# Kernel optimization log

Hardware: AMD Instinct MI355X
Metric: run time of the kernel (lower is better)

Reference implementation:

```python
import jax, jax.numpy as jnp
import numpy as np

EMBED_DIM = 128
NUM_HEADS = 4
HEAD_DIM = EMBED_DIM // NUM_HEADS


def setup_inputs() -> dict:
    key = jax.random.key(0)
    ks = jax.random.split(key, 12)
    B, N, D = 4, 4096, EMBED_DIM
    s = 1.0 / np.sqrt(D)
    inp = {
        "query": jax.random.normal(ks[0], (B, N, D), dtype=jnp.float32),
        "key": jax.random.normal(ks[1], (B, N, D), dtype=jnp.float32),
        "value": jax.random.normal(ks[2], (B, N, D), dtype=jnp.float32),
        "Wq": jax.random.uniform(ks[3], (D, D), jnp.float32, -s, s),
        "bq": jax.random.uniform(ks[4], (D,), jnp.float32, -s, s),
        "Wk": jax.random.uniform(ks[5], (D, D), jnp.float32, -s, s),
        "bk": jax.random.uniform(ks[6], (D,), jnp.float32, -s, s),
        "Wv": jax.random.uniform(ks[7], (D, D), jnp.float32, -s, s),
        "bv": jax.random.uniform(ks[8], (D,), jnp.float32, -s, s),
        "Wo": jax.random.uniform(ks[9], (D, D), jnp.float32, -s, s),
        "bo": jax.random.uniform(ks[10], (D,), jnp.float32, -s, s),
    }
    return inp


def reference(query, key, value, Wq, bq, Wk, bk, Wv, bv, Wo, bo):
    B, N, D = query.shape
    H, Dh = NUM_HEADS, HEAD_DIM
    scale = Dh ** -0.5
    # Linear projections (torch Linear: x @ W.T + b), split heads -> [B, H, N, Dh]
    Q = (query @ Wq.T + bq).reshape(B, N, H, Dh).transpose(0, 2, 1, 3)
    K = (key @ Wk.T + bk).reshape(B, N, H, Dh).transpose(0, 2, 1, 3)
    V = (value @ Wv.T + bv).reshape(B, N, H, Dh).transpose(0, 2, 1, 3)
    # Attention scores [B, H, N, N]
    scores = jnp.einsum('bhqd,bhkd->bhqk', Q, K) * scale
    attn = jax.nn.softmax(scores, axis=-1)
    ctx = jnp.einsum('bhqk,bhkd->bhqd', attn, V)  # [B, H, N, Dh]
    ctx = ctx.transpose(0, 2, 1, 3).reshape(B, N, D)
    return ctx @ Wo.T + bo
```

## Files before the change

kernel.cpp:

```cpp
#include <hip/hip_runtime.h>
#include <hip/hip_bf16.h>

#define N_SEQ 4096
#define DIM   128
#define NH    4
#define DH    32
#define BATCH 4

#define QSCALE 0.25503495870989204f

typedef __bf16 bf16x8 __attribute__((ext_vector_type(8)));
typedef __bf16 bf16x2 __attribute__((ext_vector_type(2)));
typedef __bf16 bf16x4 __attribute__((ext_vector_type(4)));
typedef float  f32x4  __attribute__((ext_vector_type(4)));

#define MFMA(a, b, c) __builtin_amdgcn_mfma_f32_16x16x32_bf16((a), (b), (c), 0, 0, 0)

static __device__ __forceinline__ bf16x8 cvt8(const float* __restrict__ p) {
    const float4* f4 = reinterpret_cast<const float4*>(p);
    float4 a = f4[0], b = f4[1];
    bf16x8 r;
    r[0] = (__bf16)a.x; r[1] = (__bf16)a.y; r[2] = (__bf16)a.z; r[3] = (__bf16)a.w;
    r[4] = (__bf16)b.x; r[5] = (__bf16)b.y; r[6] = (__bf16)b.z; r[7] = (__bf16)b.w;
    return r;
}

static __device__ __forceinline__ f32x4 exp4(f32x4 s) {
    f32x4 r;
    r[0] = __builtin_amdgcn_exp2f(s[0]);
    r[1] = __builtin_amdgcn_exp2f(s[1]);
    r[2] = __builtin_amdgcn_exp2f(s[2]);
    r[3] = __builtin_amdgcn_exp2f(s[3]);
    return r;
}

static __device__ __forceinline__ bf16x8 pack8(f32x4 a, f32x4 b) {
    bf16x8 o;
    o[0] = (__bf16)a[0]; o[1] = (__bf16)a[1];
    o[2] = (__bf16)a[2]; o[3] = (__bf16)a[3];
    o[4] = (__bf16)b[0]; o[5] = (__bf16)b[1];
    o[6] = (__bf16)b[2]; o[7] = (__bf16)b[3];
    return o;
}

__global__ __launch_bounds__(256) void proj_qkv(
    const float* __restrict__ xq, const float* __restrict__ xk, const float* __restrict__ xv,
    const float* __restrict__ Wq, const float* __restrict__ Wk, const float* __restrict__ Wv,
    const float* __restrict__ bq, const float* __restrict__ bk, const float* __restrict__ bv,
    __bf16* __restrict__ Qs, __bf16* __restrict__ Kb, __bf16* __restrict__ Vt)
{
    __shared__ __align__(16) char wlds[34816];
    const int z = blockIdx.z;
    const float* x    = (z == 0) ? xq : ((z == 1) ? xk : xv);
    const float* Wf   = (z == 0) ? Wq : ((z == 1) ? Wk : Wv);
    const float* bias = (z == 0) ? bq : ((z == 1) ? bk : bv);
    const int b    = blockIdx.y;
    const int tid  = threadIdx.x;
    const int wave = tid >> 6, lane = tid & 63;
    const int quad = lane >> 4, l15 = lane & 15;
    const int n0   = blockIdx.x * 64 + wave * 16;

    {
        const int r = tid >> 1, half = tid & 1;
        const float* wsrc = Wf + r * DIM + half * 64;
        char* wdst = wlds + r * 272 + half * 128;
        #pragma unroll
        for (int i = 0; i < 8; i++)
            *(bf16x8*)(wdst + i * 16) = cvt8(wsrc + i * 8);
    }

    bf16x8 a[4];
    const float* xrow = x + (b * N_SEQ + n0 + l15) * DIM + quad * 8;
    a[0] = cvt8(xrow);      a[1] = cvt8(xrow + 32);
    a[2] = cvt8(xrow + 64); a[3] = cvt8(xrow + 96);
    __syncthreads();

    const int n = n0 + l15;
    for (int t = 0; t < 8; t++) {
        const char* wr = wlds + (t * 16 + l15) * 272 + quad * 16;
        bf16x8 w0 = *(const bf16x8*)(wr);
        bf16x8 w1 = *(const bf16x8*)(wr + 64);
        bf16x8 w2 = *(const bf16x8*)(wr + 128);
        bf16x8 w3 = *(const bf16x8*)(wr + 192);

        f32x4 acc = {0.f, 0.f, 0.f, 0.f};
        acc = MFMA(w0, a[0], acc);
        acc = MFMA(w1, a[1], acc);
        acc = MFMA(w2, a[2], acc);
        acc = MFMA(w3, a[3], acc);

        const int d0 = t * 16 + quad * 4;
        if (z == 0) {
            const int h = d0 >> 5, dh0 = d0 & 31;
            bf16x4 q4;
            #pragma unroll
            for (int r = 0; r < 4; r++)
                q4[r] = (__bf16)((acc[r] + bias[d0 + r]) * QSCALE);
            *(bf16x4*)(Qs + ((b * NH + h) * N_SEQ + n) * DH + dh0) = q4;
        } else if (z == 1) {
            const int h = d0 >> 5, dh0 = d0 & 31;
            bf16x4 k4;
            #pragma unroll
            for (int r = 0; r < 4; r++)
                k4[r] = (__bf16)(acc[r] + bias[d0 + r]);
            *(bf16x4*)(Kb + ((b * NH + h) * N_SEQ + n) * DH + dh0) = k4;
        } else {
            const int nl = n & 63;
            const int np = (n & ~63) | (nl & 35) | ((nl & 12) << 1) | ((nl & 16) >> 2);
            #pragma unroll
            for (int r = 0; r < 4; r++) {
                const int d = d0 + r, h = d >> 5, dh = d & 31;
                Vt[((b * NH + h) * DH + dh) * N_SEQ + np] = (__bf16)(acc[r] + bias[d]);
            }
        }
    }
}

__global__ __launch_bounds__(256, 2) void flash_attn(
    const __bf16* __restrict__ Qs, const __bf16* __restrict__ Kb,
    const __bf16* __restrict__ Vt, __bf16* __restrict__ ctxb)
{
    __shared__ __align__(16) char smem[20480];
    char* const Kbase = smem;
    char* const Vbase = smem + 10240;

    const int bid  = blockIdx.x;
    const int bh   = bid & 15;
    const int qc   = bid >> 4;
    const int tid  = threadIdx.x;
    const int wave = tid >> 6, lane = tid & 63;
    const int quad = lane >> 4, l15 = lane & 15;
    const int n0   = qc * 128 + wave * 32;

    const __bf16* Qp = Qs + (bh * N_SEQ + n0) * DH;
    bf16x8 qf0 = *(const bf16x8*)(Qp + l15 * DH + quad * 8);
    bf16x8 qf1 = *(const bf16x8*)(Qp + (16 + l15) * DH + quad * 8);

    const int r_ = tid >> 2, c_ = tid & 3;
    const __bf16* gK = Kb + (size_t)bh * N_SEQ * DH + r_ * DH + c_ * 8;
    const int vd = ((r_ >> 4) & 1) * 16 + (r_ & 15);
    const int vg = r_ >> 5;
    const __bf16* gV = Vt + ((size_t)bh * DH + vd) * N_SEQ + vg * 32 + c_ * 8;
    const int kofs = r_ * 80 + c_ * 16;

    {
        bf16x8 kr = *(const bf16x8*)(gK);
        bf16x8 vr = *(const bf16x8*)(gV);
        *(bf16x8*)(Kbase + kofs) = kr;
        *(bf16x8*)(Vbase + kofs) = vr;
    }
    __syncthreads();

    f32x4 c00 = {0.f,0.f,0.f,0.f}, c01 = {0.f,0.f,0.f,0.f};
    f32x4 c10 = {0.f,0.f,0.f,0.f}, c11 = {0.f,0.f,0.f,0.f};
    f32x4 lac0 = {0.f,0.f,0.f,0.f}, lac1 = {0.f,0.f,0.f,0.f};
    const f32x4 z4 = {0.f,0.f,0.f,0.f};
    bf16x8 ones;
    #pragma unroll
    for (int i = 0; i < 8; i++) ones[i] = (__bf16)1.0f;

    for (int kb = 0; kb < N_SEQ / 64; kb++) {
        const int cur = kb & 1;
        const char* Kc = Kbase + cur * 5120;
        const char* Vc = Vbase + cur * 5120;

        const int kn = (kb + 1) & (N_SEQ / 64 - 1);
        bf16x8 krn = *(const bf16x8*)(gK + kn * 64 * DH);
        bf16x8 vrn = *(const bf16x8*)(gV + kn * 64);

        bf16x8 kf0 = *(const bf16x8*)(Kc + l15 * 80 + quad * 16);
        bf16x8 kf1 = *(const bf16x8*)(Kc + (16 + l15) * 80 + quad * 16);
        bf16x8 kf2 = *(const bf16x8*)(Kc + (32 + l15) * 80 + quad * 16);
        bf16x8 kf3 = *(const bf16x8*)(Kc + (48 + l15) * 80 + quad * 16);

        f32x4 s00 = MFMA(kf0, qf0, z4), s10 = MFMA(kf1, qf0, z4);
        f32x4 s20 = MFMA(kf2, qf0, z4), s30 = MFMA(kf3, qf0, z4);
        f32x4 s01 = MFMA(kf0, qf1, z4), s11 = MFMA(kf1, qf1, z4);
        f32x4 s21 = MFMA(kf2, qf1, z4), s31 = MFMA(kf3, qf1, z4);

        bf16x8 pf00 = pack8(exp4(s00), exp4(s10));
        bf16x8 pf10 = pack8(exp4(s20), exp4(s30));
        bf16x8 pf01 = pack8(exp4(s01), exp4(s11));
        bf16x8 pf11 = pack8(exp4(s21), exp4(s31));

        lac0 = MFMA(ones, pf00, lac0); lac0 = MFMA(ones, pf10, lac0);
        lac1 = MFMA(ones, pf01, lac1); lac1 = MFMA(ones, pf11, lac1);

        bf16x8 vf00 = *(const bf16x8*)(Vc + l15 * 80 + quad * 16);
        bf16x8 vf10 = *(const bf16x8*)(Vc + (16 + l15) * 80 + quad * 16);
        bf16x8 vf01 = *(const bf16x8*)(Vc + (32 + l15) * 80 + quad * 16);
        bf16x8 vf11 = *(const bf16x8*)(Vc + (48 + l15) * 80 + quad * 16);

        c00 = MFMA(vf00, pf00, c00); c01 = MFMA(vf10, pf00, c01);
        c00 = MFMA(vf01, pf10, c00); c01 = MFMA(vf11, pf10, c01);
        c10 = MFMA(vf00, pf01, c10); c11 = MFMA(vf10, pf01, c11);
        c10 = MFMA(vf01, pf11, c10); c11 = MFMA(vf11, pf11, c11);

        *(bf16x8*)(Kbase + (cur ^ 1) * 5120 + kofs) = krn;
        *(bf16x8*)(Vbase + (cur ^ 1) * 5120 + kofs) = vrn;
        __syncthreads();
    }

    const float inv0 = 1.0f / lac0[0];
    const float inv1 = 1.0f / lac1[0];

    const int b = bh >> 2, h = bh & 3;
    #pragma unroll
    for (int qt = 0; qt < 2; qt++) {
        const float inv = qt ? inv1 : inv0;
        const int q = n0 + qt * 16 + l15;
        #pragma unroll
        for (int dt = 0; dt < 2; dt++) {
            f32x4 cc = qt ? (dt ? c11 : c10) : (dt ? c01 : c00);
            __bf16* dst = ctxb + ((size_t)(b * N_SEQ + q)) * DIM + h * DH + dt * 16 + quad * 4;
            bf16x2 e0 = {(__bf16)(cc[0] * inv), (__bf16)(cc[1] * inv)};
            bf16x2 e1 = {(__bf16)(cc[2] * inv), (__bf16)(cc[3] * inv)};
            *(bf16x2*)(dst)     = e0;
            *(bf16x2*)(dst + 2) = e1;
        }
    }
}

__global__ __launch_bounds__(256) void out_proj(
    const __bf16* __restrict__ ctxb, const float* __restrict__ Wo,
    const float* __restrict__ bo, float* __restrict__ out)
{
    __shared__ __align__(16) char wlds[34816];
    const int b    = blockIdx.y;
    const int tid  = threadIdx.x;
    const int wave = tid >> 6, lane = tid & 63;
    const int quad = lane >> 4, l15 = lane & 15;
    const int n0   = blockIdx.x * 64 + wave * 16;

    {
        const int r = tid >> 1, half = tid & 1;
        const float* wsrc = Wo + r * DIM + half * 64;
        char* wdst = wlds + r * 272 + half * 128;
        #pragma unroll
        for (int i = 0; i < 8; i++)
            *(bf16x8*)(wdst + i * 16) = cvt8(wsrc + i * 8);
    }

    bf16x8 a[4];
    const __bf16* crow = ctxb + (b * N_SEQ + n0 + l15) * DIM + quad * 8;
    a[0] = *(const bf16x8*)(crow);
    a[1] = *(const bf16x8*)(crow + 32);
    a[2] = *(const bf16x8*)(crow + 64);
    a[3] = *(const bf16x8*)(crow + 96);
    __syncthreads();

    const int n = n0 + l15;
    for (int t = 0; t < 8; t++) {
        const char* wr = wlds + (t * 16 + l15) * 272 + quad * 16;
        bf16x8 w0 = *(const bf16x8*)(wr);
        bf16x8 w1 = *(const bf16x8*)(wr + 64);
        bf16x8 w2 = *(const bf16x8*)(wr + 128);
        bf16x8 w3 = *(const bf16x8*)(wr + 192);

        f32x4 acc = {0.f, 0.f, 0.f, 0.f};
        acc = MFMA(w0, a[0], acc);
        acc = MFMA(w1, a[1], acc);
        acc = MFMA(w2, a[2], acc);
        acc = MFMA(w3, a[3], acc);

        const int d0 = t * 16 + quad * 4;
        float4 o;
        o.x = acc[0] + bo[d0];
        o.y = acc[1] + bo[d0 + 1];
        o.z = acc[2] + bo[d0 + 2];
        o.w = acc[3] + bo[d0 + 3];
        *(float4*)(out + (b * N_SEQ + n) * DIM + d0) = o;
    }
}

extern "C" void kernel_launch(void* const* d_in, const int* in_sizes, int n_in,
                              void* d_out, int out_size, void* d_ws, size_t ws_size,
                              hipStream_t stream)
{
    const float* query = (const float*)d_in[0];
    const float* key   = (const float*)d_in[1];
    const float* value = (const float*)d_in[2];
    const float* Wq = (const float*)d_in[3];
    const float* bq = (const float*)d_in[4];
    const float* Wk = (const float*)d_in[5];
    const float* bk = (const float*)d_in[6];
    const float* Wv = (const float*)d_in[7];
    const float* bv = (const float*)d_in[8];
    const float* Wo = (const float*)d_in[9];
    const float* bo = (const float*)d_in[10];
    float* out = (float*)d_out;

    char* ws = (char*)d_ws;
    const size_t e = (size_t)BATCH * N_SEQ * DIM;
    __bf16* Qs   = (__bf16*)(ws);
    __bf16* Kb   = (__bf16*)(ws + 2 * e);
    __bf16* Vt   = (__bf16*)(ws + 4 * e);
    __bf16* ctxb = (__bf16*)(ws + 6 * e);

    proj_qkv<<<dim3(64, BATCH, 3), 256, 0, stream>>>(
        query, key, value, Wq, Wk, Wv, bq, bk, bv, Qs, Kb, Vt);
    flash_attn<<<dim3(512), 256, 0, stream>>>(Qs, Kb, Vt, ctxb);
    out_proj<<<dim3(64, BATCH), 256, 0, stream>>>(ctxb, Wo, bo, out);
}
```

Before: 160.2 us.

## Split key range across wave pairs with 64-query tiles and LDS reduction

Flash attention now gives each wave 64 query rows instead of 32. The four waves are split into two query halves times two key halves, and each key half walks 2048 keys. Partial context and row sums are merged through LDS at the end, and the row-sum MFMA with a ones vector is replaced by scalar adds plus lane shuffles. The aim is to reuse each K/V fragment across more queries and to halve the serial loop length, at the cost of more LDS (57 KB, which may limit occupancy to fewer blocks per CU), more registers and an extra reduction step.

Result: faster. 150.2 us (-6.3%).

```diff
diff --git a/kernel.cpp b/kernel.cpp
--- a/kernel.cpp
+++ b/kernel.cpp
@@ -120,9 +120,10 @@
     const __bf16* __restrict__ Qs, const __bf16* __restrict__ Kb,
     const __bf16* __restrict__ Vt, __bf16* __restrict__ ctxb)
 {
-    __shared__ __align__(16) char smem[20480];
+    __shared__ __align__(16) char smem[57344];
     char* const Kbase = smem;
-    char* const Vbase = smem + 10240;
+    char* const Vbase = smem + 20480;
+    char* const Pbase = smem + 38912;
 
     const int bid  = blockIdx.x;
     const int bh   = bid & 15;
@@ -130,93 +131,128 @@
     const int tid  = threadIdx.x;
     const int wave = tid >> 6, lane = tid & 63;
     const int quad = lane >> 4, l15 = lane & 15;
-    const int n0   = qc * 128 + wave * 32;
+    const int qh   = wave & 1, kh = wave >> 1;
+    const int n0   = qc * 128 + qh * 64;
 
     const __bf16* Qp = Qs + (bh * N_SEQ + n0) * DH;
-    bf16x8 qf0 = *(const bf16x8*)(Qp + l15 * DH + quad * 8);
-    bf16x8 qf1 = *(const bf16x8*)(Qp + (16 + l15) * DH + quad * 8);
+    bf16x8 qf[4];
+    #pragma unroll
+    for (int q = 0; q < 4; q++)
+        qf[q] = *(const bf16x8*)(Qp + (q * 16 + l15) * DH + quad * 8);
 
     const int r_ = tid >> 2, c_ = tid & 3;
     const __bf16* gK = Kb + (size_t)bh * N_SEQ * DH + r_ * DH + c_ * 8;
-    const int vd = ((r_ >> 4) & 1) * 16 + (r_ & 15);
-    const int vg = r_ >> 5;
-    const __bf16* gV = Vt + ((size_t)bh * DH + vd) * N_SEQ + vg * 32 + c_ * 8;
-    const int kofs = r_ * 80 + c_ * 16;
+    const __bf16* gV = Vt + ((size_t)bh * DH + (tid >> 3)) * N_SEQ + (tid & 7) * 8;
+    const int kofsK = r_ * 80 + c_ * 16;
+    const int kofsV = (tid >> 3) * 144 + (tid & 7) * 16;
+    const int KH = 2048;
 
     {
-        bf16x8 kr = *(const bf16x8*)(gK);
-        bf16x8 vr = *(const bf16x8*)(gV);
-        *(bf16x8*)(Kbase + kofs) = kr;
-        *(bf16x8*)(Vbase + kofs) = vr;
+        bf16x8 k0 = *(const bf16x8*)(gK);
+        bf16x8 k1 = *(const bf16x8*)(gK + (size_t)KH * DH);
+        bf16x8 v0 = *(const bf16x8*)(gV);
+        bf16x8 v1 = *(const bf16x8*)(gV + KH);
+        *(bf16x8*)(Kbase + kofsK)          = k0;
+        *(bf16x8*)(Kbase + 10240 + kofsK)  = k1;
+        *(bf16x8*)(Vbase + kofsV)          = v0;
+        *(bf16x8*)(Vbase + 9216 + kofsV)   = v1;
     }
     __syncthreads();
 
-    f32x4 c00 = {0.f,0.f,0.f,0.f}, c01 = {0.f,0.f,0.f,0.f};
-    f32x4 c10 = {0.f,0.f,0.f,0.f}, c11 = {0.f,0.f,0.f,0.f};
-    f32x4 lac0 = {0.f,0.f,0.f,0.f}, lac1 = {0.f,0.f,0.f,0.f};
+    char* const Kme = Kbase + kh * 10240;
+    char* const Vme = Vbase + kh * 9216;
+
+    f32x4 c[4][2];
+    #pragma unroll
+    for (int q = 0; q < 4; q++) { c[q][0] = f32x4{0.f,0.f,0.f,0.f}; c[q][1] = f32x4{0.f,0.f,0.f,0.f}; }
+    float l[4] = {0.f, 0.f, 0.f, 0.f};
     const f32x4 z4 = {0.f,0.f,0.f,0.f};
-    bf16x8 ones;
-    #pragma unroll
-    for (int i = 0; i < 8; i++) ones[i] = (__bf16)1.0f;
-
-    for (int kb = 0; kb < N_SEQ / 64; kb++) {
+
+    for (int kb = 0; kb < KH / 64; kb++) {
         const int cur = kb & 1;
-        const char* Kc = Kbase + cur * 5120;
-        const char* Vc = Vbase + cur * 5120;
-
-        const int kn = (kb + 1) & (N_SEQ / 64 - 1);
-        bf16x8 krn = *(const bf16x8*)(gK + kn * 64 * DH);
-        bf16x8 vrn = *(const bf16x8*)(gV + kn * 64);
+        const char* Kc = Kme + cur * 5120;
+        const char* Vc = Vme + cur * 4608;
+
+        const int kn = (kb + 1) & (KH / 64 - 1);
+        bf16x8 krn0 = *(const bf16x8*)(gK + (size_t)(kn * 64) * DH);
+        bf16x8 krn1 = *(const bf16x8*)(gK + (size_t)(KH + kn * 64) * DH);
+        bf16x8 vrn0 = *(const bf16x8*)(gV + kn * 64);
+        bf16x8 vrn1 = *(const bf16x8*)(gV + KH + kn * 64);
 
         bf16x8 kf0 = *(const bf16x8*)(Kc + l15 * 80 + quad * 16);
         bf16x8 kf1 = *(const bf16x8*)(Kc + (16 + l15) * 80 + quad * 16);
         bf16x8 kf2 = *(const bf16x8*)(Kc + (32 + l15) * 80 + quad * 16);
         bf16x8 kf3 = *(const bf16x8*)(Kc + (48 + l15) * 80 + quad * 16);
 
-        f32x4 s00 = MFMA(kf0, qf0, z4), s10 = MFMA(kf1, qf0, z4);
-        f32x4 s20 = MFMA(kf2, qf0, z4), s30 = MFMA(kf3, qf0, z4);
-        f32x4 s01 = MFMA(kf0, qf1, z4), s11 = MFMA(kf1, qf1, z4);
-        f32x4 s21 = MFMA(kf2, qf1, z4), s31 = MFMA(kf3, qf1, z4);
-
-        bf16x8 pf00 = pack8(exp4(s00), exp4(s10));
-        bf16x8 pf10 = pack8(exp4(s20), exp4(s30));
-        bf16x8 pf01 = pack8(exp4(s01), exp4(s11));
-        bf16x8 pf11 = pack8(exp4(s21), exp4(s31));
-
-        lac0 = MFMA(ones, pf00, lac0); lac0 = MFMA(ones, pf10, lac0);
-        lac1 = MFMA(ones, pf01, lac1); lac1 = MFMA(ones, pf11, lac1);
-
-        bf16x8 vf00 = *(const bf16x8*)(Vc + l15 * 80 + quad * 16);
-        bf16x8 vf10 = *(const bf16x8*)(Vc + (16 + l15) * 80 + quad * 16);
-        bf16x8 vf01 = *(const bf16x8*)(Vc + (32 + l15) * 80 + quad * 16);
-        bf16x8 vf11 = *(const bf16x8*)(Vc + (48 + l15) * 80 + quad * 16);
-
-        c00 = MFMA(vf00, pf00, c00); c01 = MFMA(vf10, pf00, c01);
-        c00 = MFMA(vf01, pf10, c00); c01 = MFMA(vf11, pf10, c01);
-        c10 = MFMA(vf00, pf01, c10); c11 = MFMA(vf10, pf01, c11);
-        c10 = MFMA(vf01, pf11, c10); c11 = MFMA(vf11, pf11, c11);
-
-        *(bf16x8*)(Kbase + (cur ^ 1) * 5120 + kofs) = krn;
-        *(bf16x8*)(Vbase + (cur ^ 1) * 5120 + kofs) = vrn;
+        bf16x8 pf[4][2];
+        #pragma unroll
+        for (int q = 0; q < 4; q++) {
+            f32x4 sa = MFMA(kf0, qf[q], z4);
+            f32x4 sb = MFMA(kf1, qf[q], z4);
+            f32x4 sc = MFMA(kf2, qf[q], z4);
+            f32x4 sd = MFMA(kf3, qf[q], z4);
+            f32x4 ea = exp4(sa), eb = exp4(sb), ec = exp4(sc), ed = exp4(sd);
+            l[q] += ((ea[0]+ea[1])+(ea[2]+ea[3])) + ((eb[0]+eb[1])+(eb[2]+eb[3]))
+                  + ((ec[0]+ec[1])+(ec[2]+ec[3])) + ((ed[0]+ed[1])+(ed[2]+ed[3]));
+            pf[q][0] = pack8(ea, eb);
+            pf[q][1] = pack8(ec, ed);
+        }
+
+        bf16x8 vf00 = *(const bf16x8*)(Vc + l15 * 144 + quad * 16);
+        bf16x8 vf10 = *(const bf16x8*)(Vc + (16 + l15) * 144 + quad * 16);
+        bf16x8 vf01 = *(const bf16x8*)(Vc + l15 * 144 + 64 + quad * 16);
+        bf16x8 vf11 = *(const bf16x8*)(Vc + (16 + l15) * 144 + 64 + quad * 16);
+
+        #pragma unroll
+        for (int q = 0; q < 4; q++) {
+            c[q][0] = MFMA(vf00, pf[q][0], c[q][0]);
+            c[q][1] = MFMA(vf10, pf[q][0], c[q][1]);
+            c[q][0] = MFMA(vf01, pf[q][1], c[q][0]);
+            c[q][1] = MFMA(vf11, pf[q][1], c[q][1]);
+        }
+
+        *(bf16x8*)(Kbase + (cur ^ 1) * 5120 + kofsK)          = krn0;
+        *(bf16x8*)(Kbase + 10240 + (cur ^ 1) * 5120 + kofsK)  = krn1;
+        *(bf16x8*)(Vbase + (cur ^ 1) * 4608 + kofsV)          = vrn0;
+        *(bf16x8*)(Vbase + 9216 + (cur ^ 1) * 4608 + kofsV)   = vrn1;
         __syncthreads();
     }
 
-    const float inv0 = 1.0f / lac0[0];
-    const float inv1 = 1.0f / lac1[0];
-
-    const int b = bh >> 2, h = bh & 3;
     #pragma unroll
-    for (int qt = 0; qt < 2; qt++) {
-        const float inv = qt ? inv1 : inv0;
-        const int q = n0 + qt * 16 + l15;
-        #pragma unroll
-        for (int dt = 0; dt < 2; dt++) {
-            f32x4 cc = qt ? (dt ? c11 : c10) : (dt ? c01 : c00);
-            __bf16* dst = ctxb + ((size_t)(b * N_SEQ + q)) * DIM + h * DH + dt * 16 + quad * 4;
-            bf16x2 e0 = {(__bf16)(cc[0] * inv), (__bf16)(cc[1] * inv)};
-            bf16x2 e1 = {(__bf16)(cc[2] * inv), (__bf16)(cc[3] * inv)};
-            *(bf16x2*)(dst)     = e0;
-            *(bf16x2*)(dst + 2) = e1;
+    for (int q = 0; q < 4; q++) {
+        l[q] += __shfl_xor(l[q], 16);
+        l[q] += __shfl_xor(l[q], 32);
+    }
+
+    char* const Pme = Pbase + qh * 9216 + lane * 144;
+    if (kh == 1) {
+        #pragma unroll
+        for (int q = 0; q < 4; q++) {
+            *(f32x4*)(Pme + (q * 2 + 0) * 16) = c[q][0];
+            *(f32x4*)(Pme + (q * 2 + 1) * 16) = c[q][1];
+        }
+        f32x4 lv = {l[0], l[1], l[2], l[3]};
+        *(f32x4*)(Pme + 128) = lv;
+    }
+    __syncthreads();
+    if (kh == 0) {
+        f32x4 lp = *(const f32x4*)(Pme + 128);
+        const int b = bh >> 2, h = bh & 3;
+        #pragma unroll
+        for (int q = 0; q < 4; q++) {
+            c[q][0] += *(const f32x4*)(Pme + (q * 2 + 0) * 16);
+            c[q][1] += *(const f32x4*)(Pme + (q * 2 + 1) * 16);
+            const float inv = 1.0f / (l[q] + lp[q]);
+            const int qg = n0 + q * 16 + l15;
+            __bf16* dst = ctxb + ((size_t)(b * N_SEQ + qg)) * DIM + h * DH + quad * 4;
+            #pragma unroll
+            for (int dt = 0; dt < 2; dt++) {
+                f32x4 cc = c[q][dt];
+                bf16x2 e0 = {(__bf16)(cc[0] * inv), (__bf16)(cc[1] * inv)};
+                bf16x2 e1 = {(__bf16)(cc[2] * inv), (__bf16)(cc[3] * inv)};
+                *(bf16x2*)(dst + dt * 16)     = e0;
+                *(bf16x2*)(dst + dt * 16 + 2) = e1;
+            }
         }
     }
 }
```
